# Kernel optimization log

Hardware: AMD Instinct MI355X
Metric: run time of the kernel (lower is better)

The kernel has to match this reference:

```python
import jax, jax.numpy as jnp
import numpy as np

SR = 44100  # sample_rate from __init__


def setup_inputs() -> dict:
    key = jax.random.key(0)
    k1, k2 = jax.random.split(key)
    x = jax.random.normal(k1, (64, 2, 131072), dtype=jnp.float32) * 0.1
    t = jax.random.uniform(k2, (64,), dtype=jnp.float32)
    filter_freq = jnp.array([1000.0], dtype=jnp.float32)  # learnable param
    filter_q = jnp.array([0.707], dtype=jnp.float32)      # learnable param
    return {"x": x, "t": t, "filter_freq": filter_freq, "filter_q": filter_q}


def _highpass_biquad(x, filter_freq, filter_q):
    # parameter clamping as in the module's forward
    freq = jnp.clip(filter_freq, 100.0, SR / 2.0 - 1.0)[0]
    q = jnp.clip(filter_q, 0.1, 10.0)[0]
    # torchaudio highpass_biquad coefficients
    w0 = 2.0 * jnp.pi * freq / SR
    cosw = jnp.cos(w0)
    alpha = jnp.sin(w0) / (2.0 * q)
    a0 = 1.0 + alpha
    b0 = ((1.0 + cosw) * 0.5) / a0
    b1 = (-(1.0 + cosw)) / a0
    b2 = b0
    a1 = (-2.0 * cosw) / a0
    a2 = (1.0 - alpha) / a0
    # FIR (feedforward) part, zero initial conditions: fused elementwise
    x1 = jnp.pad(x, ((0, 0), (0, 0), (1, 0)))[..., :-1]
    x2 = jnp.pad(x, ((0, 0), (0, 0), (2, 0)))[..., :-2]
    xf = b0 * x + b1 * x1 + b2 * x2  # [B, C, T]
    # IIR (feedback) 2nd-order recurrence over time, vectorized over (B, C)
    xf_t = jnp.moveaxis(xf, -1, 0)  # [T, B, C]

    def step(carry, u):
        y1, y2 = carry
        y = u - a1 * y1 - a2 * y2
        return (y, y1), y

    zero = jnp.zeros(xf_t.shape[1:], xf_t.dtype)
    _, ys = jax.lax.scan(step, (zero, zero), xf_t)
    y = jnp.moveaxis(ys, 0, -1)  # [B, C, T]
    # torchaudio lfilter default clamp=True
    return jnp.clip(y, -1.0, 1.0)


def reference(x, t, filter_freq, filter_q):
    # t is accepted but unused, matching the original forward signature
    return _highpass_biquad(x, filter_freq, filter_q)
```

## Files before the change

kernel.cpp:

```cpp
#include <hip/hip_runtime.h>
#include <math.h>


constexpr int T_LEN  = 131072;
constexpr int RLEN   = 8192;
constexpr int BATCH  = 256;
constexpr int NBATCH = RLEN / BATCH;
constexpr int REG_PER_SEQ = T_LEN / RLEN;
constexpr int NSEQ   = 128;
constexpr int NBLOCKS = NSEQ * REG_PER_SEQ;

typedef float fx4 __attribute__((ext_vector_type(4)));

#define MATSQ(d00,d01,d10,d11, s00,s01,s10,s11) { \
    d00 = fmaf(s00, s00, s01 * s10); \
    d01 = fmaf(s00, s01, s01 * s11); \
    d10 = fmaf(s10, s00, s11 * s10); \
    d11 = fmaf(s10, s01, s11 * s11); }

__global__ __launch_bounds__(64) void hp_kernel(
    const float* __restrict__ x,
    const float* __restrict__ pfreq,
    const float* __restrict__ pq,
    float* __restrict__ out)
{
    float freq = fminf(fmaxf(pfreq[0], 100.0f), 44100.0f * 0.5f - 1.0f);
    float q    = fminf(fmaxf(pq[0], 0.1f), 10.0f);
    float w0   = 2.0f * (float)M_PI * freq / 44100.0f;
    float cw   = cosf(w0);
    float alpha = sinf(w0) / (2.0f * q);
    float ia0  = 1.0f / (1.0f + alpha);
    const float b0 = (1.0f + cw) * 0.5f * ia0;
    const float b1 = -(1.0f + cw) * ia0;
    const float b2 = b0;
    const float a1 = -2.0f * cw * ia0;
    const float a2 = (1.0f - alpha) * ia0;

    float t00, t01, t10, t11;
    MATSQ(t00,t01,t10,t11, -a1, -a2, 1.f, 0.f);
    float u100,u101,u110,u111; MATSQ(u100,u101,u110,u111, t00,t01,t10,t11);
    float u200,u201,u210,u211; MATSQ(u200,u201,u210,u211, u100,u101,u110,u111);
    float u400,u401,u410,u411; MATSQ(u400,u401,u410,u411, u200,u201,u210,u211);
    float u800,u801,u810,u811; MATSQ(u800,u801,u810,u811, u400,u401,u410,u411);
    float uG00,uG01,uG10,uG11; MATSQ(uG00,uG01,uG10,uG11, u800,u801,u810,u811);
    float uH00,uH01,uH10,uH11; MATSQ(uH00,uH01,uH10,uH11, uG00,uG01,uG10,uG11);

    const int borig = blockIdx.x;
    const int b     = ((borig & 7) << 8) | (borig >> 3);

    const int seq = b >> 4;
    const int S   = (b & (REG_PER_SEQ - 1)) * RLEN;
    const float* __restrict__ xs = x   + (size_t)seq * T_LEN;
    float*       __restrict__ os = out + (size_t)seq * T_LEN;
    const int tid = threadIdx.x;

    const fx4* gx = (const fx4*)xs;
    fx4*       go = (fx4*)os;
    const int  base4 = S >> 2;

    float by1 = 0.f, by2 = 0.f;
    float bxm1 = 0.f, bxm2 = 0.f;
    if (S > 0 && tid == 0) {
        bxm1 = xs[S - BATCH - 1];
        bxm2 = xs[S - BATCH - 2];
    }

    const int startB = (S > 0) ? -1 : 0;

    fx4 v = gx[base4 + startB * 64 + tid];

#pragma unroll 2
    for (int j = startB; j < NBATCH; ++j) {
        fx4 vc = v;
        if (j + 1 < NBATCH)
            v = gx[base4 + (j + 1) * 64 + tid];

        float pm1 = __shfl_up(vc.w, 1);
        float pm2 = __shfl_up(vc.z, 1);
        float xm1 = (tid == 0) ? bxm1 : pm1;
        float xm2 = (tid == 0) ? bxm2 : pm2;
        float xf0 = fmaf(b0, vc.x, fmaf(b1, xm1,  b2 * xm2));
        float xf1 = fmaf(b0, vc.y, fmaf(b1, vc.x, b2 * xm1));
        float xf2 = fmaf(b0, vc.z, fmaf(b1, vc.y, b2 * vc.x));
        float xf3 = fmaf(b0, vc.w, fmaf(b1, vc.z, b2 * vc.y));

        float c0 = xf0, c1 = 0.f;
        float nc;
        nc = fmaf(-a1, c0, fmaf(-a2, c1, xf1)); c1 = c0; c0 = nc;
        nc = fmaf(-a1, c0, fmaf(-a2, c1, xf2)); c1 = c0; c0 = nc;
        nc = fmaf(-a1, c0, fmaf(-a2, c1, xf3)); c1 = c0; c0 = nc;

        {
            float i0 = fmaf(u100, by1, fmaf(u101, by2, c0));
            float i1 = fmaf(u110, by1, fmaf(u111, by2, c1));
            c0 = (tid == 0) ? i0 : c0;
            c1 = (tid == 0) ? i1 : c1;
        }

#define SCAN_LVL(D, U00, U01, U10, U11) { \
        float pc0 = __shfl_up(c0, D), pc1 = __shfl_up(c1, D); \
        float n0 = fmaf(U00, pc0, fmaf(U01, pc1, c0)); \
        float n1 = fmaf(U10, pc0, fmaf(U11, pc1, c1)); \
        if (tid >= D) { c0 = n0; c1 = n1; } }
        SCAN_LVL(1,  u100,u101,u110,u111)
        SCAN_LVL(2,  u200,u201,u210,u211)
        SCAN_LVL(4,  u400,u401,u410,u411)
        SCAN_LVL(8,  u800,u801,u810,u811)
        SCAN_LVL(16, uG00,uG01,uG10,uG11)
        SCAN_LVL(32, uH00,uH01,uH10,uH11)
#undef SCAN_LVL

        float yi1 = __shfl_up(c0, 1);
        float yi2 = __shfl_up(c1, 1);
        yi1 = (tid == 0) ? by1 : yi1;
        yi2 = (tid == 0) ? by2 : yi2;

        float y0 = fmaf(-a1, yi1, fmaf(-a2, yi2, xf0));
        float y1v = fmaf(-a1, y0,  fmaf(-a2, yi1, xf1));
        float y2v = fmaf(-a1, y1v, fmaf(-a2, y0,  xf2));
        float y3v = fmaf(-a1, y2v, fmaf(-a2, y1v, xf3));

        by1  = __shfl(c0, 63);
        by2  = __shfl(c1, 63);
        bxm1 = __shfl(vc.w, 63);
        bxm2 = __shfl(vc.z, 63);

        if (j >= 0) {
            fx4 o;
            o.x = fminf(fmaxf(y0,  -1.f), 1.f);
            o.y = fminf(fmaxf(y1v, -1.f), 1.f);
            o.z = fminf(fmaxf(y2v, -1.f), 1.f);
            o.w = fminf(fmaxf(y3v, -1.f), 1.f);
            __builtin_nontemporal_store(o, &go[base4 + j * 64 + tid]);
        }
    }
}

extern "C" void kernel_launch(void* const* d_in, const int* in_sizes, int n_in,
                              void* d_out, int out_size, void* d_ws, size_t ws_size,
                              hipStream_t stream) {
    const float* x  = (const float*)d_in[0];
    const float* ff = (const float*)d_in[2];
    const float* fq = (const float*)d_in[3];
    float* out = (float*)d_out;
    hp_kernel<<<NBLOCKS, 64, 0, stream>>>(x, ff, fq, out);
}
```

Baseline: 127.4 us.

## Halve region length and restructure wave scan with precomputed per-lane carry matrices

Region length drops from 8192 to 4096 samples, doubling the number of blocks and halving each block's serial batch loop. The warmup batch now makes up a larger share of each block's work. The in-batch scan now runs on local prefixes only, with the last shuffle level dropped. Each lane applies the incoming batch carry through a precomputed per-lane power matrix Q, and the carry is advanced using the 256-step matrix. This shortens the serial dependency chain per batch at the cost of a few extra FMAs, and it relies on the low-precision-tolerant warmup for cross-region state.

```diff
diff --git a/kernel.cpp b/kernel.cpp
--- a/kernel.cpp
+++ b/kernel.cpp
@@ -3,7 +3,7 @@
 
 
 constexpr int T_LEN  = 131072;
-constexpr int RLEN   = 8192;
+constexpr int RLEN   = 4096;
 constexpr int BATCH  = 256;
 constexpr int NBATCH = RLEN / BATCH;
 constexpr int REG_PER_SEQ = T_LEN / RLEN;
@@ -44,21 +44,38 @@
     float u800,u801,u810,u811; MATSQ(u800,u801,u810,u811, u400,u401,u410,u411);
     float uG00,uG01,uG10,uG11; MATSQ(uG00,uG01,uG10,uG11, u800,u801,u810,u811);
     float uH00,uH01,uH10,uH11; MATSQ(uH00,uH01,uH10,uH11, uG00,uG01,uG10,uG11);
+    float r00, r01, r10, r11;  MATSQ(r00,r01,r10,r11,     uH00,uH01,uH10,uH11);
+
+    const int tid = threadIdx.x;
+
+    float Q00 = 1.f, Q01 = 0.f, Q10 = 0.f, Q11 = 1.f;
+#define QMUL(BIT, U00,U01,U10,U11) if (tid & BIT) { \
+        float n00 = fmaf(U00, Q00, U01 * Q10); \
+        float n01 = fmaf(U00, Q01, U01 * Q11); \
+        float n10 = fmaf(U10, Q00, U11 * Q10); \
+        float n11 = fmaf(U10, Q01, U11 * Q11); \
+        Q00 = n00; Q01 = n01; Q10 = n10; Q11 = n11; }
+    QMUL(1,  u100,u101,u110,u111)
+    QMUL(2,  u200,u201,u210,u211)
+    QMUL(4,  u400,u401,u410,u411)
+    QMUL(8,  u800,u801,u810,u811)
+    QMUL(16, uG00,uG01,uG10,uG11)
+    QMUL(32, uH00,uH01,uH10,uH11)
+#undef QMUL
 
     const int borig = blockIdx.x;
-    const int b     = ((borig & 7) << 8) | (borig >> 3);
+    const int b     = ((borig & 7) << 9) | (borig >> 3);
 
-    const int seq = b >> 4;
+    const int seq = b >> 5;
     const int S   = (b & (REG_PER_SEQ - 1)) * RLEN;
     const float* __restrict__ xs = x   + (size_t)seq * T_LEN;
     float*       __restrict__ os = out + (size_t)seq * T_LEN;
-    const int tid = threadIdx.x;
 
     const fx4* gx = (const fx4*)xs;
     fx4*       go = (fx4*)os;
     const int  base4 = S >> 2;
 
-    float by1 = 0.f, by2 = 0.f;
+    float e0 = 0.f, e1 = 0.f;
     float bxm1 = 0.f, bxm2 = 0.f;
     if (S > 0 && tid == 0) {
         bxm1 = xs[S - BATCH - 1];
@@ -90,13 +107,6 @@
         nc = fmaf(-a1, c0, fmaf(-a2, c1, xf2)); c1 = c0; c0 = nc;
         nc = fmaf(-a1, c0, fmaf(-a2, c1, xf3)); c1 = c0; c0 = nc;
 
-        {
-            float i0 = fmaf(u100, by1, fmaf(u101, by2, c0));
-            float i1 = fmaf(u110, by1, fmaf(u111, by2, c1));
-            c0 = (tid == 0) ? i0 : c0;
-            c1 = (tid == 0) ? i1 : c1;
-        }
-
 #define SCAN_LVL(D, U00, U01, U10, U11) { \
         float pc0 = __shfl_up(c0, D), pc1 = __shfl_up(c1, D); \
         float n0 = fmaf(U00, pc0, fmaf(U01, pc1, c0)); \
@@ -107,21 +117,23 @@
         SCAN_LVL(4,  u400,u401,u410,u411)
         SCAN_LVL(8,  u800,u801,u810,u811)
         SCAN_LVL(16, uG00,uG01,uG10,uG11)
-        SCAN_LVL(32, uH00,uH01,uH10,uH11)
 #undef SCAN_LVL
 
-        float yi1 = __shfl_up(c0, 1);
-        float yi2 = __shfl_up(c1, 1);
-        yi1 = (tid == 0) ? by1 : yi1;
-        yi2 = (tid == 0) ? by2 : yi2;
+        float pc0 = __shfl_up(c0, 1);
+        float pc1 = __shfl_up(c1, 1);
+        float yi1 = (tid == 0) ? e0 : fmaf(Q00, e0, fmaf(Q01, e1, pc0));
+        float yi2 = (tid == 0) ? e1 : fmaf(Q10, e0, fmaf(Q11, e1, pc1));
 
-        float y0 = fmaf(-a1, yi1, fmaf(-a2, yi2, xf0));
+        float y0  = fmaf(-a1, yi1, fmaf(-a2, yi2, xf0));
         float y1v = fmaf(-a1, y0,  fmaf(-a2, yi1, xf1));
         float y2v = fmaf(-a1, y1v, fmaf(-a2, y0,  xf2));
         float y3v = fmaf(-a1, y2v, fmaf(-a2, y1v, xf3));
 
-        by1  = __shfl(c0, 63);
-        by2  = __shfl(c1, 63);
+        float s630 = __shfl(c0, 63);
+        float s631 = __shfl(c1, 63);
+        float ne0 = fmaf(r00, e0, fmaf(r01, e1, s630));
+        float ne1 = fmaf(r10, e0, fmaf(r11, e1, s631));
+        e0 = ne0; e1 = ne1;
         bxm1 = __shfl(vc.w, 63);
         bxm2 = __shfl(vc.z, 63);
 
```

New measurement: 120.6 us. 1.06x faster.
